# Performance work log

Hardware: AMD Instinct MI355X
Metric: run time of the kernel (lower is better)

Reference implementation:

```python
import jax, jax.numpy as jnp
import numpy as np

K = 9  # 3x3 kernel taps

def conv2d(x, w, b):
    # stride 1, padding 1, NCHW / OIHW
    out = jax.lax.conv_general_dilated(x, w, (1, 1), ((1, 1), (1, 1)),
                                       dimension_numbers=('NCHW', 'OIHW', 'NCHW'))
    return out + b[None, :, None, None]

def deform_conv2d(x, offset, mask, w, b):
    # torchvision modulated deformable conv, kernel 3x3, stride 1, pad 1, dilation 1
    B, C, H, W = x.shape
    off = offset.reshape(B, K, 2, H, W)  # per-tap (dy, dx)
    ii = (jnp.arange(K) // 3).astype(x.dtype) - 1.0  # kernel row offset (pad=1)
    jj = (jnp.arange(K) % 3).astype(x.dtype) - 1.0   # kernel col offset
    hh = jnp.arange(H, dtype=x.dtype)[None, None, :, None]
    ww = jnp.arange(W, dtype=x.dtype)[None, None, None, :]
    py = hh + ii[None, :, None, None] + off[:, :, 0]  # [B,K,H,W] sample rows
    px = ww + jj[None, :, None, None] + off[:, :, 1]  # [B,K,H,W] sample cols

    y0 = jnp.floor(py); x0 = jnp.floor(px)
    dy = py - y0; dx = px - x0
    y0 = y0.astype(jnp.int32); x0 = x0.astype(jnp.int32)

    xf = x.reshape(B, C, H * W)

    def gather(yi, xi):
        valid = ((yi >= 0) & (yi < H) & (xi >= 0) & (xi < W)).astype(x.dtype)
        yc = jnp.clip(yi, 0, H - 1)
        xc = jnp.clip(xi, 0, W - 1)
        idx = (yc * W + xc).reshape(B, K * H * W)
        v = jax.vmap(lambda xb, ib: xb[:, ib])(xf, idx)  # [B,C,K*H*W]
        return v.reshape(B, C, K, H, W) * valid[:, None]

    v00 = gather(y0,     x0)
    v01 = gather(y0,     x0 + 1)
    v10 = gather(y0 + 1, x0)
    v11 = gather(y0 + 1, x0 + 1)

    dy = dy[:, None]; dx = dx[:, None]  # broadcast over channel dim
    val = (v00 * (1 - dy) * (1 - dx) + v01 * (1 - dy) * dx
           + v10 * dy * (1 - dx) + v11 * dy * dx)
    val = val * mask[:, None]  # sigmoid modulation, [B,1,K,H,W]

    out = jnp.einsum('ock,bckhw->bohw', w.reshape(w.shape[0], C, K), val)
    return out + b[None, :, None, None]

def setup_inputs() -> dict:
    key = jax.random.key(0)
    k1, k2, k3 = jax.random.split(key, 3)
    x = jax.random.normal(k1, (8, 3, 512, 512), dtype=jnp.float32)
    w_off = jax.random.normal(k2, (27, 3, 3, 3), dtype=jnp.float32) * 0.05
    b_off = jnp.zeros((27,), dtype=jnp.float32)
    w_def = jax.random.normal(k3, (3, 3, 3, 3), dtype=jnp.float32) * 0.1
    b_def = jnp.zeros((3,), dtype=jnp.float32)
    return {'x': x, 'w_off': w_off, 'b_off': b_off, 'w_def': w_def, 'b_def': b_def}

def reference(x, w_off, b_off, w_def, b_def):
    ow = conv2d(x, w_off, b_off)            # [B,27,H,W]
    offset = ow[:, :18]                      # 2*9 offsets
    mask = jax.nn.sigmoid(ow[:, 18:])        # 9 modulation masks
    return deform_conv2d(x, offset, mask, w_def, b_def)
```

## Files before the change

kernel.cpp:

```cpp
#include <hip/hip_runtime.h>
#include <math.h>

typedef float f2 __attribute__((ext_vector_type(2)));
typedef float f2u __attribute__((ext_vector_type(2), aligned(4)));
typedef float f4 __attribute__((ext_vector_type(4)));

#define BN 8
#define CIN 3
#define HH 512
#define WW 512
#define KK 9
#define PATCH 27

__global__ void reorder_weights(const float* __restrict__ w_off,
                                const float* __restrict__ b_off,
                                const float* __restrict__ w_def,
                                float* __restrict__ ws)
{
    for (int idx = threadIdx.x; idx < 928; idx += blockDim.x) {
        float v = 0.0f;
        if (idx < 756) {
            const int i = idx / 28, r = idx % 28;
            const int q = r >> 1, half = r & 1;
            if (q < 13)      v = w_off[(2 * q + half) * PATCH + i];
            else if (!half)  v = w_off[26 * PATCH + i];
        } else if (idx < 900) {
            const int t = idx - 756;
            const int k = t / 16, r = t % 16;
            if (r < 12) {
                const int c = r >> 2, o = r & 3;
                if (o < 3) v = w_def[o * PATCH + c * KK + k];
            } else if (r == 12) v = b_off[2 * k];
            else if (r == 13)   v = b_off[2 * k + 1];
            else if (r == 14)   v = b_off[18 + k];
        } else {
            const int r = idx - 900;
            const int q = r >> 1, half = r & 1;
            if (q < 13)      v = b_off[2 * q + half];
            else if (!half)  v = b_off[26];
        }
        ws[idx] = v;
    }
}

__global__ __launch_bounds__(256) void deform_fused_kernel(
    const float* __restrict__ x,
    const float* __restrict__ wsw,
    const float* __restrict__ b_def,
    float* __restrict__ out)
{
    const int w = blockIdx.x * blockDim.x + threadIdx.x;
    const int h = blockIdx.y;
    const int b = blockIdx.z;

    const size_t plane = (size_t)HH * WW;
    const float* xb = x + (size_t)b * CIN * plane;

    float patch[PATCH];
    #pragma unroll
    for (int c = 0; c < CIN; ++c) {
        const float* xp = xb + c * plane;
        #pragma unroll
        for (int t = 0; t < KK; ++t) {
            const int yy = h + t / 3 - 1;
            const int xx = w + t % 3 - 1;
            const bool in = ((unsigned)yy < HH) & ((unsigned)xx < WW);
            const int yc = min(max(yy, 0), HH - 1);
            const int xc = min(max(xx, 0), WW - 1);
            patch[c * KK + t] = in ? xp[yc * WW + xc] : 0.0f;
        }
    }

    f2 ow[14];
    #pragma unroll
    for (int q = 0; q < 14; ++q) ow[q] = *(const f2*)(wsw + 900 + 2 * q);

    #pragma unroll
    for (int i = 0; i < PATCH; ++i) {
        const float p = patch[i];
        const f2 pp = { p, p };
        const f4* row = (const f4*)(wsw + i * 28);
        #pragma unroll
        for (int j = 0; j < 7; ++j) {
            const f4 wq = row[j];
            const f2 lo = { wq.x, wq.y };
            const f2 hi = { wq.z, wq.w };
            ow[2 * j]     = __builtin_elementwise_fma(lo, pp, ow[2 * j]);
            ow[2 * j + 1] = __builtin_elementwise_fma(hi, pp, ow[2 * j + 1]);
        }
    }

    f2 acc01 = { b_def[0], b_def[1] };
    float acc2 = b_def[2];

    #pragma unroll
    for (int k = 0; k < KK; ++k) {
        const float* blk = wsw + 756 + k * 16;

        const float oy = ow[k].x;
        const float ox = ow[k].y;
        const float om = (k < 8) ? ((k & 1) ? ow[9 + (k >> 1)].y
                                            : ow[9 + (k >> 1)].x)
                                 : ow[13].x;

        const float m = __builtin_amdgcn_rcpf(1.0f + __expf(-om));

        const float py = (float)h + (float)(k / 3 - 1) + oy;
        const float px = (float)w + (float)(k % 3 - 1) + ox;
        const float y0f = floorf(py);
        const float x0f = floorf(px);
        const float dy = py - y0f;
        const float dx = px - x0f;
        const int y0 = (int)y0f;
        const int x0 = (int)x0f;

        const int xL = min(max(x0, 0), WW - 2);
        const float w0p = 1.0f - dx;
        const float w1p = dx;
        const bool P = (x0 == xL);
        const bool Q = (x0 + 1 == xL);
        const bool R = (x0 - 1 == xL);
        const float wa = P ? w0p : (Q ? w1p : 0.0f);
        const float wb = P ? w1p : (R ? w0p : 0.0f);

        const int yc0 = min(max(y0, 0), HH - 1);
        const int yc1 = min(max(y0 + 1, 0), HH - 1);
        const float ady = ((unsigned)y0 < HH)       ? (1.0f - dy) * m : 0.0f;
        const float bdy = ((unsigned)(y0 + 1) < HH) ? dy * m          : 0.0f;

        const f2 wxp = { wa, wb };
        const f2 wTe = wxp * ady;
        const f2 wBe = wxp * bdy;

        const int off0 = yc0 * WW + xL;
        const int off1 = yc1 * WW + xL;

        #pragma unroll
        for (int c = 0; c < CIN; ++c) {
            const float* xp = xb + c * plane;
            const f2 vT = *(const f2u*)(xp + off0);
            const f2 vB = *(const f2u*)(xp + off1);
            f2 s = vT * wTe;
            s = __builtin_elementwise_fma(vB, wBe, s);
            const float val = s.x + s.y;
            const f4 wq = *(const f4*)(blk + 4 * c);
            const f2 w01 = { wq.x, wq.y };
            const f2 vv = { val, val };
            acc01 = __builtin_elementwise_fma(w01, vv, acc01);
            acc2 = fmaf(wq.z, val, acc2);
        }
    }

    const size_t base = (size_t)b * (CIN * plane) + (size_t)h * WW + w;
    out[base]             = acc01.x;
    out[base + plane]     = acc01.y;
    out[base + 2 * plane] = acc2;
}

extern "C" void kernel_launch(void* const* d_in, const int* in_sizes, int n_in,
                              void* d_out, int out_size, void* d_ws, size_t ws_size,
                              hipStream_t stream) {
    const float* x     = (const float*)d_in[0];
    const float* w_off = (const float*)d_in[1];
    const float* b_off = (const float*)d_in[2];
    const float* w_def = (const float*)d_in[3];
    const float* b_def = (const float*)d_in[4];
    float* out = (float*)d_out;
    float* wsw = (float*)d_ws;

    reorder_weights<<<1, 256, 0, stream>>>(w_off, b_off, w_def, wsw);

    dim3 block(256, 1, 1);
    dim3 grid(WW / 256, HH, BN);
    deform_fused_kernel<<<grid, block, 0, stream>>>(x, wsw, b_def, out);
}
```

Before: 191.9 us.

## Compute offset/mask conv with bf16 MFMA via per-wave LDS staging

The 27-output offset/mask convolution is replaced with bf16 MFMA 16x16x32 instructions. Each thread writes its 3x3x3 patch, padded with a bias-one column, to shared memory as bf16. The MFMA results are written back to shared memory and each thread reads its own 27 outputs. Weights are pre-packed into an MFMA A-fragment layout with the bias folded in. This swaps the scalar FMA chain for matrix instructions and LDS round-trips, but rounding the inputs and weights to bf16 reduces precision of the offsets and masks, which can move sample positions.

Measured after the change: 241.5 us. 1.26x slower.

```diff
diff --git a/kernel.cpp b/kernel.cpp
--- a/kernel.cpp
+++ b/kernel.cpp
@@ -1,9 +1,12 @@
 #include <hip/hip_runtime.h>
+#include <hip/hip_bf16.h>
 #include <math.h>
 
 typedef float f2 __attribute__((ext_vector_type(2)));
 typedef float f2u __attribute__((ext_vector_type(2), aligned(4)));
 typedef float f4 __attribute__((ext_vector_type(4)));
+typedef short s8v __attribute__((ext_vector_type(8)));
+typedef unsigned int u4 __attribute__((ext_vector_type(4)));
 
 #define BN 8
 #define CIN 3
@@ -15,48 +18,56 @@
 __global__ void reorder_weights(const float* __restrict__ w_off,
                                 const float* __restrict__ b_off,
                                 const float* __restrict__ w_def,
-                                float* __restrict__ ws)
+                                void* __restrict__ ws)
 {
-    for (int idx = threadIdx.x; idx < 928; idx += blockDim.x) {
+    unsigned short* wsA = (unsigned short*)ws;
+    float* wsf = (float*)((char*)ws + 2048);
+    const int tid = threadIdx.x;
+    for (int idx = tid; idx < 1024; idx += blockDim.x) {
+        const int ct = idx >> 9;
+        const int L  = (idx >> 3) & 63;
+        const int j  = idx & 7;
+        const int m = ct * 16 + (L & 15);
+        const int k = (L >> 4) * 8 + j;
         float v = 0.0f;
-        if (idx < 756) {
-            const int i = idx / 28, r = idx % 28;
-            const int q = r >> 1, half = r & 1;
-            if (q < 13)      v = w_off[(2 * q + half) * PATCH + i];
-            else if (!half)  v = w_off[26 * PATCH + i];
-        } else if (idx < 900) {
-            const int t = idx - 756;
-            const int k = t / 16, r = t % 16;
-            if (r < 12) {
-                const int c = r >> 2, o = r & 3;
-                if (o < 3) v = w_def[o * PATCH + c * KK + k];
-            } else if (r == 12) v = b_off[2 * k];
-            else if (r == 13)   v = b_off[2 * k + 1];
-            else if (r == 14)   v = b_off[18 + k];
-        } else {
-            const int r = idx - 900;
-            const int q = r >> 1, half = r & 1;
-            if (q < 13)      v = b_off[2 * q + half];
-            else if (!half)  v = b_off[26];
-        }
-        ws[idx] = v;
+        if (m < PATCH) {
+            if (k < PATCH)       v = w_off[m * PATCH + k];
+            else if (k == PATCH) v = b_off[m];
+        }
+        __hip_bfloat16 hv = __float2bfloat16(v);
+        wsA[idx] = *(unsigned short*)&hv;
+    }
+    for (int idx = tid; idx < 144; idx += blockDim.x) {
+        const int k = idx / 16, r = idx % 16;
+        float v = 0.0f;
+        if (r < 12) {
+            const int c = r >> 2, o = r & 3;
+            if (o < 3) v = w_def[o * PATCH + c * KK + k];
+        }
+        wsf[idx] = v;
     }
 }
 
 __global__ __launch_bounds__(256) void deform_fused_kernel(
     const float* __restrict__ x,
-    const float* __restrict__ wsw,
+    const void* __restrict__ ws,
     const float* __restrict__ b_def,
     float* __restrict__ out)
 {
-    const int w = blockIdx.x * blockDim.x + threadIdx.x;
+    __shared__ __attribute__((aligned(16))) char smem[4][9216];
+    const int tid = threadIdx.x;
+    const int lane = tid & 63;
+    char* base = smem[tid >> 6];
+
+    const int w = blockIdx.x * blockDim.x + tid;
     const int h = blockIdx.y;
     const int b = blockIdx.z;
 
     const size_t plane = (size_t)HH * WW;
     const float* xb = x + (size_t)b * CIN * plane;
 
-    float patch[PATCH];
+    float pf[28];
+    pf[27] = 1.0f;
     #pragma unroll
     for (int c = 0; c < CIN; ++c) {
         const float* xp = xb + c * plane;
@@ -67,35 +78,65 @@
             const bool in = ((unsigned)yy < HH) & ((unsigned)xx < WW);
             const int yc = min(max(yy, 0), HH - 1);
             const int xc = min(max(xx, 0), WW - 1);
-            patch[c * KK + t] = in ? xp[yc * WW + xc] : 0.0f;
-        }
-    }
+            pf[c * KK + t] = in ? xp[yc * WW + xc] : 0.0f;
+        }
+    }
+
+    unsigned u[16];
+    #pragma unroll
+    for (int pr = 0; pr < 14; ++pr) {
+        union { __hip_bfloat162 h2; unsigned uu; } cv;
+        cv.h2 = __float22bfloat162_rn(make_float2(pf[2 * pr], pf[2 * pr + 1]));
+        u[pr] = cv.uu;
+    }
+    u[14] = 0u; u[15] = 0u;
+    #pragma unroll
+    for (int j = 0; j < 4; ++j) {
+        u4 q = { u[4 * j], u[4 * j + 1], u[4 * j + 2], u[4 * j + 3] };
+        *(u4*)(base + lane * 72 + j * 16) = q;
+    }
+    asm volatile("s_waitcnt lgkmcnt(0)" ::: "memory");
+
+    const s8v* wsA = (const s8v*)ws;
+    const s8v a0 = wsA[lane];
+    const s8v a1 = wsA[64 + lane];
+
+    const int colp = lane & 15;
+    const int quad = lane >> 4;
+    s8v bfr[4];
+    #pragma unroll
+    for (int T = 0; T < 4; ++T)
+        bfr[T] = *(const s8v*)(base + (T * 16 + colp) * 72 + quad * 16);
+
+    __builtin_amdgcn_sched_barrier(0);
+
+    const f4 zz = { 0.0f, 0.0f, 0.0f, 0.0f };
+    #pragma unroll
+    for (int T = 0; T < 4; ++T) {
+        f4 c0 = __builtin_amdgcn_mfma_f32_16x16x32_bf16(a0, bfr[T], zz, 0, 0, 0);
+        f4 c1 = __builtin_amdgcn_mfma_f32_16x16x32_bf16(a1, bfr[T], zz, 0, 0, 0);
+        char* prow = base + (T * 16 + colp) * 144;
+        *(f4*)(prow + (quad * 4) * 4)        = c0;
+        *(f4*)(prow + (16 + quad * 4) * 4)   = c1;
+    }
+    asm volatile("s_waitcnt lgkmcnt(0)" ::: "memory");
 
     f2 ow[14];
     #pragma unroll
-    for (int q = 0; q < 14; ++q) ow[q] = *(const f2*)(wsw + 900 + 2 * q);
-
-    #pragma unroll
-    for (int i = 0; i < PATCH; ++i) {
-        const float p = patch[i];
-        const f2 pp = { p, p };
-        const f4* row = (const f4*)(wsw + i * 28);
-        #pragma unroll
-        for (int j = 0; j < 7; ++j) {
-            const f4 wq = row[j];
-            const f2 lo = { wq.x, wq.y };
-            const f2 hi = { wq.z, wq.w };
-            ow[2 * j]     = __builtin_elementwise_fma(lo, pp, ow[2 * j]);
-            ow[2 * j + 1] = __builtin_elementwise_fma(hi, pp, ow[2 * j + 1]);
-        }
-    }
+    for (int q = 0; q < 7; ++q) {
+        const f4 v = *(const f4*)(base + lane * 144 + q * 16);
+        ow[2 * q]     = (f2){ v.x, v.y };
+        ow[2 * q + 1] = (f2){ v.z, v.w };
+    }
+
+    const float* wsf = (const float*)((const char*)ws + 2048);
 
     f2 acc01 = { b_def[0], b_def[1] };
     float acc2 = b_def[2];
 
     #pragma unroll
     for (int k = 0; k < KK; ++k) {
-        const float* blk = wsw + 756 + k * 16;
+        const float* blk = wsf + k * 16;
 
         const float oy = ow[k].x;
         const float ox = ow[k].y;
@@ -151,10 +192,10 @@
         }
     }
 
-    const size_t base = (size_t)b * (CIN * plane) + (size_t)h * WW + w;
-    out[base]             = acc01.x;
-    out[base + plane]     = acc01.y;
-    out[base + 2 * plane] = acc2;
+    const size_t obase = (size_t)b * (CIN * plane) + (size_t)h * WW + w;
+    out[obase]             = acc01.x;
+    out[obase + plane]     = acc01.y;
+    out[obase + 2 * plane] = acc2;
 }
 
 extern "C" void kernel_launch(void* const* d_in, const int* in_sizes, int n_in,
@@ -166,11 +207,10 @@
     const float* w_def = (const float*)d_in[3];
     const float* b_def = (const float*)d_in[4];
     float* out = (float*)d_out;
-    float* wsw = (float*)d_ws;
-
-    reorder_weights<<<1, 256, 0, stream>>>(w_off, b_off, w_def, wsw);
+
+    reorder_weights<<<1, 256, 0, stream>>>(w_off, b_off, w_def, d_ws);
 
     dim3 block(256, 1, 1);
     dim3 grid(WW / 256, HH, BN);
-    deform_fused_kernel<<<grid, block, 0, stream>>>(x, wsw, b_def, out);
+    deform_fused_kernel<<<grid, block, 0, stream>>>(x, d_ws, b_def, out);
 }
```
